# Performance work log

Measured on AMD Instinct MI355X. Metric: run time of the kernel, lower is better.

Reference implementation:

```python
import jax, jax.numpy as jnp
import numpy as np

B, N, L, D, V = 32, 2048, 128, 1024, 32000

def setup_inputs() -> dict:
    key = jax.random.key(0)
    k1, k2, k3 = jax.random.split(key, 3)
    image_features = jax.random.normal(k1, (B, N, D), dtype=jnp.float32)
    token_ids = jax.random.randint(k2, (B, L), 0, V, dtype=jnp.int64)
    emb_table = jax.random.normal(k3, (V, D), dtype=jnp.float32)
    return {"image_features": image_features, "token_ids": token_ids, "emb_table": emb_table}

def reference(image_features, token_ids, emb_table):
    # targets = embeddings(input_ids): [B, L, D]
    targets = emb_table[token_ids]
    # batched pairwise L2 distance (torch.cdist p=2): ||x-y|| via the
    # expanded form ||x||^2 + ||y||^2 - 2<x,y>, clamped for numerical safety.
    x2 = jnp.sum(image_features * image_features, axis=-1)        # [B, N]
    y2 = jnp.sum(targets * targets, axis=-1)                      # [B, L]
    xy = jnp.einsum('bnd,bld->bnl', image_features, targets)      # [B, N, L]
    d2 = x2[:, :, None] + y2[:, None, :] - 2.0 * xy
    costs = jnp.sqrt(jnp.maximum(d2, 0.0))                        # [B, N, L]
    smallest = jnp.min(costs, axis=-1)                            # [B, N]
    return smallest.mean()
```

## Files before the change

kernel.cpp:

```cpp
#include <hip/hip_runtime.h>
#include <cstdint>
#include <cstddef>

#define BATCH 32
#define NROW  2048
#define LTOK  128
#define DDIM  1024

#define BM    64
#define BK    64
#define NK    (DDIM / BK)
#define LDST  72

typedef short s8v  __attribute__((ext_vector_type(8)));
typedef float f4v  __attribute__((ext_vector_type(4)));

__device__ __forceinline__ uint32_t pk2(float lo, float hi) {
    return __builtin_amdgcn_perm(__float_as_uint(hi), __float_as_uint(lo), 0x07060302u);
}

__global__ __launch_bounds__(256)
void prep_y(const int*   __restrict__ tok,
            const float* __restrict__ E,
            uint32_t*    __restrict__ Ybf,
            float*       __restrict__ y2)
{
    const int l = blockIdx.x, b = blockIdx.y;
    const int tid = threadIdx.x;
    const int t = tok[b * LTOK + l];
    const float4 v = ((const float4*)(E + (size_t)t * DDIM))[tid];
    float s = v.x*v.x + v.y*v.y + v.z*v.z + v.w*v.w;
    uint2 p; p.x = pk2(v.x, v.y); p.y = pk2(v.z, v.w);
    ((uint2*)(Ybf + ((size_t)(b * LTOK + l) * DDIM) / 2))[tid] = p;
#pragma unroll
    for (int o = 1; o < 64; o <<= 1) s += __shfl_xor(s, o);
    __shared__ float ws4[4];
    if ((tid & 63) == 0) ws4[tid >> 6] = s;
    __syncthreads();
    if (tid == 0) y2[b * LTOK + l] = ws4[0] + ws4[1] + ws4[2] + ws4[3];
}

__global__ __launch_bounds__(256, 4)
void cdist_min_mean_kernel(const float* __restrict__ X,
                           const short* __restrict__ Ybf,
                           const float* __restrict__ y2g,
                           float* __restrict__ out)
{
    __shared__ __align__(16) short Xs[2][BM * LDST];
    __shared__ float x2s[BM];
    __shared__ float rowmin[BM * 2];

    const int tid  = threadIdx.x;
    const int lane = tid & 63;
    const int wid  = tid >> 6;
    const int grp  = tid >> 3;
    const int sub  = tid & 7;

    const int b       = blockIdx.y;
    const int rowBase = blockIdx.x * BM;

    const float* Xg  = X + ((size_t)b * NROW + rowBase) * DDIM;
    const float* xp0 = Xg + (size_t)grp * DDIM + sub * 8;
    const float* xp1 = Xg + (size_t)(grp + 32) * DDIM + sub * 8;

    const int quad = lane >> 4;
    const int l15  = lane & 15;
    const int wm   = wid >> 1;
    const int wn   = wid & 1;

    const short* yb[4];
#pragma unroll
    for (int ni = 0; ni < 4; ++ni)
        yb[ni] = Ybf + (size_t)(b * LTOK + wn * 64 + ni * 16 + l15) * DDIM + quad * 8;

    f4v acc[2][4];
#pragma unroll
    for (int mi = 0; mi < 2; ++mi)
#pragma unroll
        for (int ni = 0; ni < 4; ++ni)
            acc[mi][ni] = (f4v){0.f, 0.f, 0.f, 0.f};

    float xacc[2] = {0.f, 0.f};

    float4 xra[2], xrb[2];
    s8v    yr[4][2];

    auto loadx = [&](int k) {
        xra[0] = *(const float4*)(xp0 + k * BK);
        xrb[0] = *(const float4*)(xp0 + k * BK + 4);
        xra[1] = *(const float4*)(xp1 + k * BK);
        xrb[1] = *(const float4*)(xp1 + k * BK + 4);
    };
    auto loady = [&](int k) {
#pragma unroll
        for (int ni = 0; ni < 4; ++ni)
#pragma unroll
            for (int s = 0; s < 2; ++s)
                yr[ni][s] = *(const s8v*)(yb[ni] + k * BK + s * 32);
    };
    auto pack = [&](int dst) {
#pragma unroll
        for (int i = 0; i < 2; ++i) {
            const float4 a = xra[i], c = xrb[i];
            xacc[i] += a.x*a.x + a.y*a.y + a.z*a.z + a.w*a.w
                     + c.x*c.x + c.y*c.y + c.z*c.z + c.w*c.w;
            uint4 p;
            p.x = pk2(a.x, a.y); p.y = pk2(a.z, a.w);
            p.z = pk2(c.x, c.y); p.w = pk2(c.z, c.w);
            *(uint4*)&Xs[dst][(grp + 32 * i) * LDST + sub * 8] = p;
        }
    };

    loadx(0);
    pack(0);
    loadx(1);
    loady(0);
    __syncthreads();

#pragma unroll
    for (int k = 0; k < NK; ++k) {
        const int buf = k & 1;
        if (k < NK - 1) pack(buf ^ 1);
        if (k < NK - 2) loadx(k + 2);
#pragma unroll
        for (int ks = 0; ks < 2; ++ks) {
            s8v af[2];
#pragma unroll
            for (int mi = 0; mi < 2; ++mi)
                af[mi] = *(const s8v*)&Xs[buf][(wm * 32 + mi * 16 + l15) * LDST + ks * 32 + quad * 8];
#pragma unroll
            for (int mi = 0; mi < 2; ++mi)
#pragma unroll
                for (int ni = 0; ni < 4; ++ni)
                    acc[mi][ni] = __builtin_amdgcn_mfma_f32_16x16x32_bf16(
                        af[mi], yr[ni][ks], acc[mi][ni], 0, 0, 0);
        }
        if (k < NK - 1) loady(k + 1);
        __syncthreads();
    }

#pragma unroll
    for (int i = 0; i < 2; ++i) {
        float s = xacc[i];
        s += __shfl_xor(s, 1); s += __shfl_xor(s, 2); s += __shfl_xor(s, 4);
        if ((lane & 7) == 0) x2s[grp + 32 * i] = s;
    }

    float y2r[4];
#pragma unroll
    for (int ni = 0; ni < 4; ++ni)
        y2r[ni] = y2g[b * LTOK + wn * 64 + ni * 16 + l15];

#pragma unroll
    for (int mi = 0; mi < 2; ++mi) {
#pragma unroll
        for (int j = 0; j < 4; ++j) {
            float m = y2r[0] - 2.f * acc[mi][0][j];
            m = fminf(m, y2r[1] - 2.f * acc[mi][1][j]);
            m = fminf(m, y2r[2] - 2.f * acc[mi][2][j]);
            m = fminf(m, y2r[3] - 2.f * acc[mi][3][j]);
            m = fminf(m, __shfl_xor(m, 1));
            m = fminf(m, __shfl_xor(m, 2));
            m = fminf(m, __shfl_xor(m, 4));
            m = fminf(m, __shfl_xor(m, 8));
            if (l15 == 0)
                rowmin[(wm * 32 + mi * 16 + quad * 4 + j) * 2 + wn] = m;
        }
    }
    __syncthreads();

    if (tid < BM) {
        float m = fminf(rowmin[tid * 2], rowmin[tid * 2 + 1]);
        float part = sqrtf(fmaxf(x2s[tid] + m, 0.f));
#pragma unroll
        for (int s = 1; s < 64; s <<= 1) part += __shfl_xor(part, s);
        if (lane == 0)
            atomicAdd(out, part * (1.0f / (float)(BATCH * NROW)));
    }
}

extern "C" void kernel_launch(void* const* d_in, const int* in_sizes, int n_in,
                              void* d_out, int out_size, void* d_ws, size_t ws_size,
                              hipStream_t stream) {
    const float* X   = (const float*)d_in[0];
    const int*   tok = (const int*)d_in[1];
    const float* E   = (const float*)d_in[2];
    float* out = (float*)d_out;

    uint32_t* Ybf = (uint32_t*)d_ws;
    float*    y2  = (float*)((char*)d_ws + (size_t)BATCH * LTOK * DDIM * 2);

    hipMemsetAsync(out, 0, sizeof(float), stream);

    dim3 pgrid(LTOK, BATCH, 1);
    prep_y<<<pgrid, 256, 0, stream>>>(tok, E, Ybf, y2);

    dim3 grid(NROW / BM, BATCH, 1);
    cdist_min_mean_kernel<<<grid, 256, 0, stream>>>(X, (const short*)Ybf, y2, out);
}
```

Baseline: 466.3 us.

## Stage Y tiles in LDS via direct global loads, keep X fragments in registers

```diff
diff --git a/kernel.cpp b/kernel.cpp
--- a/kernel.cpp
+++ b/kernel.cpp
@@ -6,11 +6,6 @@
 #define NROW  2048
 #define LTOK  128
 #define DDIM  1024
-
-#define BM    64
-#define BK    64
-#define NK    (DDIM / BK)
-#define LDST  72
 
 typedef short s8v  __attribute__((ext_vector_type(8)));
 typedef float f4v  __attribute__((ext_vector_type(4)));
@@ -46,135 +41,107 @@
                            const float* __restrict__ y2g,
                            float* __restrict__ out)
 {
-    __shared__ __align__(16) short Xs[2][BM * LDST];
-    __shared__ float x2s[BM];
-    __shared__ float rowmin[BM * 2];
+    __shared__ __align__(16) short Ys[LTOK * 128];
+    __shared__ float x2s[64];
+    __shared__ float rowmin[64];
 
     const int tid  = threadIdx.x;
     const int lane = tid & 63;
     const int wid  = tid >> 6;
-    const int grp  = tid >> 3;
-    const int sub  = tid & 7;
+    const int quad = lane >> 4;
+    const int l15  = lane & 15;
+    const int rxor = l15 & 7;
 
     const int b       = blockIdx.y;
-    const int rowBase = blockIdx.x * BM;
+    const int rowBase = blockIdx.x * 64;
 
-    const float* Xg  = X + ((size_t)b * NROW + rowBase) * DDIM;
-    const float* xp0 = Xg + (size_t)grp * DDIM + sub * 8;
-    const float* xp1 = Xg + (size_t)(grp + 32) * DDIM + sub * 8;
+    const float* xptr = X + ((size_t)b * NROW + rowBase + wid * 16 + l15) * DDIM + quad * 8;
 
-    const int quad = lane >> 4;
-    const int l15  = lane & 15;
-    const int wm   = wid >> 1;
-    const int wn   = wid & 1;
+    const short* ysrc = Ybf + ((size_t)b * LTOK + (tid >> 4)) * DDIM
+                      + (((tid & 15) ^ ((tid >> 4) & 7)) * 8);
 
-    const short* yb[4];
+    f4v acc[8];
 #pragma unroll
-    for (int ni = 0; ni < 4; ++ni)
-        yb[ni] = Ybf + (size_t)(b * LTOK + wn * 64 + ni * 16 + l15) * DDIM + quad * 8;
+    for (int ni = 0; ni < 8; ++ni) acc[ni] = (f4v){0.f, 0.f, 0.f, 0.f};
+    float xacc = 0.f;
 
-    f4v acc[2][4];
+    float4 pa[4], pb[4];
 #pragma unroll
-    for (int mi = 0; mi < 2; ++mi)
-#pragma unroll
-        for (int ni = 0; ni < 4; ++ni)
-            acc[mi][ni] = (f4v){0.f, 0.f, 0.f, 0.f};
-
-    float xacc[2] = {0.f, 0.f};
-
-    float4 xra[2], xrb[2];
-    s8v    yr[4][2];
-
-    auto loadx = [&](int k) {
-        xra[0] = *(const float4*)(xp0 + k * BK);
-        xrb[0] = *(const float4*)(xp0 + k * BK + 4);
-        xra[1] = *(const float4*)(xp1 + k * BK);
-        xrb[1] = *(const float4*)(xp1 + k * BK + 4);
-    };
-    auto loady = [&](int k) {
-#pragma unroll
-        for (int ni = 0; ni < 4; ++ni)
-#pragma unroll
-            for (int s = 0; s < 2; ++s)
-                yr[ni][s] = *(const s8v*)(yb[ni] + k * BK + s * 32);
-    };
-    auto pack = [&](int dst) {
-#pragma unroll
-        for (int i = 0; i < 2; ++i) {
-            const float4 a = xra[i], c = xrb[i];
-            xacc[i] += a.x*a.x + a.y*a.y + a.z*a.z + a.w*a.w
-                     + c.x*c.x + c.y*c.y + c.z*c.z + c.w*c.w;
-            uint4 p;
-            p.x = pk2(a.x, a.y); p.y = pk2(a.z, a.w);
-            p.z = pk2(c.x, c.y); p.w = pk2(c.z, c.w);
-            *(uint4*)&Xs[dst][(grp + 32 * i) * LDST + sub * 8] = p;
-        }
-    };
-
-    loadx(0);
-    pack(0);
-    loadx(1);
-    loady(0);
-    __syncthreads();
-
-#pragma unroll
-    for (int k = 0; k < NK; ++k) {
-        const int buf = k & 1;
-        if (k < NK - 1) pack(buf ^ 1);
-        if (k < NK - 2) loadx(k + 2);
-#pragma unroll
-        for (int ks = 0; ks < 2; ++ks) {
-            s8v af[2];
-#pragma unroll
-            for (int mi = 0; mi < 2; ++mi)
-                af[mi] = *(const s8v*)&Xs[buf][(wm * 32 + mi * 16 + l15) * LDST + ks * 32 + quad * 8];
-#pragma unroll
-            for (int mi = 0; mi < 2; ++mi)
-#pragma unroll
-                for (int ni = 0; ni < 4; ++ni)
-                    acc[mi][ni] = __builtin_amdgcn_mfma_f32_16x16x32_bf16(
-                        af[mi], yr[ni][ks], acc[mi][ni], 0, 0, 0);
-        }
-        if (k < NK - 1) loady(k + 1);
-        __syncthreads();
+    for (int t = 0; t < 3; ++t) {
+        pa[t] = *(const float4*)(xptr + t * 32);
+        pb[t] = *(const float4*)(xptr + t * 32 + 4);
     }
 
 #pragma unroll
-    for (int i = 0; i < 2; ++i) {
-        float s = xacc[i];
-        s += __shfl_xor(s, 1); s += __shfl_xor(s, 2); s += __shfl_xor(s, 4);
-        if ((lane & 7) == 0) x2s[grp + 32 * i] = s;
+    for (int t = 0; t < 32; ++t) {
+        if ((t & 3) == 0) {
+            const int e = t >> 2;
+            if (t) __syncthreads();
+#pragma unroll
+            for (int i = 0; i < 8; ++i)
+                __builtin_amdgcn_global_load_lds(
+                    (const __attribute__((address_space(1))) void*)
+                        (ysrc + (size_t)i * 16 * DDIM + e * 128),
+                    (__attribute__((address_space(3))) void*)
+                        &Ys[(i * 256 + (wid << 6)) * 8],
+                    16, 0, 0);
+            __syncthreads();
+        }
+
+        const float4 a = pa[t & 3], c = pb[t & 3];
+        xacc += a.x*a.x + a.y*a.y + a.z*a.z + a.w*a.w
+              + c.x*c.x + c.y*c.y + c.z*c.z + c.w*c.w;
+        uint4 p;
+        p.x = pk2(a.x, a.y); p.y = pk2(a.z, a.w);
+        p.z = pk2(c.x, c.y); p.w = pk2(c.z, c.w);
+        s8v af;
+        __builtin_memcpy(&af, &p, 16);
+
+        if (t + 3 < 32) {
+            pa[(t + 3) & 3] = *(const float4*)(xptr + (t + 3) * 32);
+            pb[(t + 3) & 3] = *(const float4*)(xptr + (t + 3) * 32 + 4);
+        }
+
+        const int ksl = t & 3;
+#pragma unroll
+        for (int ni = 0; ni < 8; ++ni) {
+            const s8v bf = *(const s8v*)&Ys[(ni * 16 + l15) * 128
+                                            + (((ksl * 4 + quad) ^ rxor) * 8)];
+            acc[ni] = __builtin_amdgcn_mfma_f32_16x16x32_bf16(af, bf, acc[ni], 0, 0, 0);
+        }
     }
 
-    float y2r[4];
+    {
+        float s = xacc;
+        s += __shfl_xor(s, 16);
+        s += __shfl_xor(s, 32);
+        if (lane < 16) x2s[wid * 16 + lane] = s;
+    }
+
+    float y2r[8];
 #pragma unroll
-    for (int ni = 0; ni < 4; ++ni)
-        y2r[ni] = y2g[b * LTOK + wn * 64 + ni * 16 + l15];
+    for (int ni = 0; ni < 8; ++ni)
+        y2r[ni] = y2g[b * LTOK + ni * 16 + l15];
 
 #pragma unroll
-    for (int mi = 0; mi < 2; ++mi) {
+    for (int j = 0; j < 4; ++j) {
+        float m = y2r[0] - 2.f * acc[0][j];
 #pragma unroll
-        for (int j = 0; j < 4; ++j) {
-            float m = y2r[0] - 2.f * acc[mi][0][j];
-            m = fminf(m, y2r[1] - 2.f * acc[mi][1][j]);
-            m = fminf(m, y2r[2] - 2.f * acc[mi][2][j]);
-            m = fminf(m, y2r[3] - 2.f * acc[mi][3][j]);
-            m = fminf(m, __shfl_xor(m, 1));
-            m = fminf(m, __shfl_xor(m, 2));
-            m = fminf(m, __shfl_xor(m, 4));
-            m = fminf(m, __shfl_xor(m, 8));
-            if (l15 == 0)
-                rowmin[(wm * 32 + mi * 16 + quad * 4 + j) * 2 + wn] = m;
-        }
+        for (int ni = 1; ni < 8; ++ni)
+            m = fminf(m, y2r[ni] - 2.f * acc[ni][j]);
+        m = fminf(m, __shfl_xor(m, 1));
+        m = fminf(m, __shfl_xor(m, 2));
+        m = fminf(m, __shfl_xor(m, 4));
+        m = fminf(m, __shfl_xor(m, 8));
+        if (l15 == 0) rowmin[wid * 16 + quad * 4 + j] = m;
     }
     __syncthreads();
 
-    if (tid < BM) {
-        float m = fminf(rowmin[tid * 2], rowmin[tid * 2 + 1]);
-        float part = sqrtf(fmaxf(x2s[tid] + m, 0.f));
+    if (tid < 64) {
+        float part = sqrtf(fmaxf(x2s[tid] + rowmin[tid], 0.f));
 #pragma unroll
         for (int s = 1; s < 64; s <<= 1) part += __shfl_xor(part, s);
-        if (lane == 0)
+        if (tid == 0)
             atomicAdd(out, part * (1.0f / (float)(BATCH * NROW)));
     }
 }
@@ -195,6 +162,6 @@
     dim3 pgrid(LTOK, BATCH, 1);
     prep_y<<<pgrid, 256, 0, stream>>>(tok, E, Ybf, y2);
 
-    dim3 grid(NROW / BM, BATCH, 1);
+    dim3 grid(NROW / 64, BATCH, 1);
     cdist_min_mean_kernel<<<grid, 256, 0, stream>>>(X, (const short*)Ybf, y2, out);
 }
```

New measurement: 427.6 us. 8.3% less time.
